# Kernel tuning notes

Hardware: AMD Instinct MI355X
Metric: run time of the kernel (lower is better)

## Reference

```python
import jax, jax.numpy as jnp
import numpy as np

EPS = 1e-5  # torch GroupNorm default

def gn1(x, g, b):
    # GroupNorm with 1 group: normalize over (C,H,W) per sample, per-channel affine
    m = jnp.mean(x, axis=(1, 2, 3), keepdims=True)
    v = jnp.var(x, axis=(1, 2, 3), keepdims=True)
    return (x - m) * jax.lax.rsqrt(v + EPS) * g[None, :, None, None] + b[None, :, None, None]

def conv1x1(x, w):
    # w: [O, C]; 1x1 conv == channel GEMM
    return jnp.einsum('bchw,oc->bohw', x, w)

def interp_bilinear_ac(x, H, W):
    # bilinear, align_corners=True
    b, c, h, w = x.shape
    ys = jnp.linspace(0.0, h - 1.0, H)
    xs = jnp.linspace(0.0, w - 1.0, W)
    y0 = jnp.floor(ys).astype(jnp.int32); y1 = jnp.minimum(y0 + 1, h - 1)
    x0 = jnp.floor(xs).astype(jnp.int32); x1 = jnp.minimum(x0 + 1, w - 1)
    wy = (ys - y0)[None, None, :, None]
    wx = (xs - x0)[None, None, None, :]
    rows = x[:, :, y0, :] * (1.0 - wy) + x[:, :, y1, :] * wy
    return rows[:, :, :, x0] * (1.0 - wx) + rows[:, :, :, x1] * wx

C, KC, NCLS = 256, 128, 21
B, H, W = 8, 128, 128

def setup_inputs() -> dict:
    key = jax.random.key(0)
    ks = jax.random.split(key, 16)
    s = 0.01  # matches torch init normal_(0, 0.01)
    d = {
        'feats': jax.random.normal(ks[0], (B, C, H, W), jnp.float32),
        'out_aux': jax.random.normal(ks[1], (B, NCLS, 64, 64), jnp.float32),
        # f_pixel: conv(C->KC), GN, relu, conv(KC->KC), GN, relu
        'fp_w1': jax.random.normal(ks[2], (KC, C), jnp.float32) * s,
        'fp_g1': jnp.ones((KC,), jnp.float32), 'fp_b1': jnp.zeros((KC,), jnp.float32),
        'fp_w2': jax.random.normal(ks[3], (KC, KC), jnp.float32) * s,
        'fp_g2': jnp.ones((KC,), jnp.float32), 'fp_b2': jnp.zeros((KC,), jnp.float32),
        # f_object
        'fo_w1': jax.random.normal(ks[4], (KC, C), jnp.float32) * s,
        'fo_g1': jnp.ones((KC,), jnp.float32), 'fo_b1': jnp.zeros((KC,), jnp.float32),
        'fo_w2': jax.random.normal(ks[5], (KC, KC), jnp.float32) * s,
        'fo_g2': jnp.ones((KC,), jnp.float32), 'fo_b2': jnp.zeros((KC,), jnp.float32),
        # f_down
        'fd_w': jax.random.normal(ks[6], (KC, C), jnp.float32) * s,
        'fd_g': jnp.ones((KC,), jnp.float32), 'fd_b': jnp.zeros((KC,), jnp.float32),
        # f_up
        'fu_w': jax.random.normal(ks[7], (C, KC), jnp.float32) * s,
        'fu_g': jnp.ones((C,), jnp.float32), 'fu_b': jnp.zeros((C,), jnp.float32),
        # conv_bn_dropout: conv(2C->C), GN, relu (dropout is identity in eval)
        'cb_w': jax.random.normal(ks[8], (C, 2 * C), jnp.float32) * s,
        'cb_g': jnp.ones((C,), jnp.float32), 'cb_b': jnp.zeros((C,), jnp.float32),
    }
    return d

def reference(feats, out_aux, fp_w1, fp_g1, fp_b1, fp_w2, fp_g2, fp_b2,
              fo_w1, fo_g1, fo_b1, fo_w2, fo_g2, fo_b2,
              fd_w, fd_g, fd_b, fu_w, fu_g, fu_b, cb_w, cb_g, cb_b):
    b, c, h, w = feats.shape
    kc = fp_w1.shape[0]
    n = h * w
    # --- SpatialGather: softmax(probs over spatial) @ feats^T -> proxy [b,c,K,1]
    probs = interp_bilinear_ac(out_aux, h, w).reshape(b, -1, n)
    probs = jax.nn.softmax(probs, axis=2)                       # [b,K,n]
    ctx = jnp.einsum('bkn,bcn->bck', probs, feats.reshape(b, c, n))[..., None]  # [b,c,K,1]
    # --- ObjectAttentionBlock2D
    q = jax.nn.relu(gn1(conv1x1(feats, fp_w1), fp_g1, fp_b1))
    q = jax.nn.relu(gn1(conv1x1(q, fp_w2), fp_g2, fp_b2)).reshape(b, kc, n)     # [b,kc,n]
    k = jax.nn.relu(gn1(conv1x1(ctx, fo_w1), fo_g1, fo_b1))
    k = jax.nn.relu(gn1(conv1x1(k, fo_w2), fo_g2, fo_b2)).reshape(b, kc, -1)    # [b,kc,K]
    v = jax.nn.relu(gn1(conv1x1(ctx, fd_w), fd_g, fd_b)).reshape(b, kc, -1)     # [b,kc,K]
    sim = jnp.einsum('bcn,bck->bnk', q, k) * (kc ** -0.5)       # [b,n,K]
    sim = jax.nn.softmax(sim, axis=-1)
    att = jnp.einsum('bnk,bck->bcn', sim, v).reshape(b, kc, h, w)
    up = jax.nn.relu(gn1(conv1x1(att, fu_w), fu_g, fu_b))       # [b,c,h,w]
    # --- fuse (dropout = identity at inference)
    cat = jnp.concatenate([up, feats], axis=1)
    return jax.nn.relu(gn1(conv1x1(cat, cb_w), cb_g, cb_b))
```

## Files before the change

### kernel.cpp

```cpp
#include <hip/hip_runtime.h>
#include <hip/hip_bf16.h>

#define BB 8
#define CC 256
#define KCH 128
#define NCLS 21
#define NN 16384
#define IH 64
#define IW 64
#define GEPS 1e-5f

typedef unsigned short u16;
typedef short v8s __attribute__((ext_vector_type(8)));
typedef u16 v8us __attribute__((ext_vector_type(8)));
typedef float v4f __attribute__((ext_vector_type(4)));

#define OFF_STATS   0u
#define OFF_CTX     64u
#define OFF_KMAT    43072u
#define OFF_VMAT    64576u
#define OFF_WB1     86080u
#define OFF_WB2     102464u
#define OFF_WB3     110656u
#define OFF_WB4     127040u
#define OFF_FEATSB  196608u
#define OFF_POOL    16973824u

__device__ __forceinline__ float bfu2f(u16 u) {
    unsigned int x = ((unsigned int)u) << 16;
    return __uint_as_float(x);
}
__device__ __forceinline__ u16 f2bfu(float f) {
    __hip_bfloat16 h = __float2bfloat16(f);
    return *reinterpret_cast<u16*>(&h);
}

__device__ __forceinline__ float blk_sum(float v, float* red) {
    #pragma unroll
    for (int o = 32; o > 0; o >>= 1) v += __shfl_down(v, o, 64);
    int lane = threadIdx.x & 63, w = threadIdx.x >> 6;
    __syncthreads();
    if (lane == 0) red[w] = v;
    __syncthreads();
    return red[0] + red[1] + red[2] + red[3];
}
__device__ __forceinline__ float blk_max(float v, float* red) {
    #pragma unroll
    for (int o = 32; o > 0; o >>= 1) v = fmaxf(v, __shfl_down(v, o, 64));
    int lane = threadIdx.x & 63, w = threadIdx.x >> 6;
    __syncthreads();
    if (lane == 0) red[w] = v;
    __syncthreads();
    return fmaxf(fmaxf(red[0], red[1]), fmaxf(red[2], red[3]));
}

__global__ __launch_bounds__(256) void conv_weights(
    const float* __restrict__ w1, const float* __restrict__ w2,
    const float* __restrict__ w3, const float* __restrict__ w4,
    u16* __restrict__ o1, u16* __restrict__ o2,
    u16* __restrict__ o3, u16* __restrict__ o4)
{
    int i = blockIdx.x * 256 + threadIdx.x;
    if (i < 32768) o1[i] = f2bfu(w1[i]);
    else if (i < 49152) o2[i - 32768] = f2bfu(w2[i - 32768]);
    else if (i < 81920) o3[i - 49152] = f2bfu(w3[i - 49152]);
    else if (i < 212992) o4[i - 81920] = f2bfu(w4[i - 81920]);
}

__global__ __launch_bounds__(256) void feats_to_nhwc(
    const float* __restrict__ feats, u16* __restrict__ outp)
{
    __shared__ float tile[64][65];
    int b = blockIdx.z, c0 = blockIdx.y * 64, n0 = blockIdx.x * 64;
    int tid = threadIdx.x, tx = tid & 63, ty = tid >> 6;
    #pragma unroll
    for (int r = 0; r < 16; r++) {
        int c = ty * 16 + r;
        tile[c][tx] = feats[((size_t)(b * CC + c0 + c)) * NN + n0 + tx];
    }
    __syncthreads();
    #pragma unroll
    for (int r = 0; r < 16; r++) {
        int nl = ty * 16 + r;
        outp[((size_t)b * NN + n0 + nl) * CC + c0 + tx] = f2bfu(tile[tx][nl]);
    }
}

__global__ __launch_bounds__(256) void interp_softmax_kernel(
    const float* __restrict__ aux, float* __restrict__ probs)
{
    int bk = blockIdx.x;
    const float* src = aux + (size_t)bk * (IH * IW);
    float* dst = probs + (size_t)bk * NN;
    int tid = threadIdx.x;
    __shared__ float red[4];
    const float scale = 63.0f / 127.0f;
    float lmax = -1e30f;
    for (int idx = tid; idx < NN; idx += 256) {
        int y = idx >> 7, x = idx & 127;
        float fy = y * scale, fx = x * scale;
        int y0 = (int)fy, x0 = (int)fx;
        float wy = fy - y0, wx = fx - x0;
        int y1 = min(y0 + 1, IH - 1), x1 = min(x0 + 1, IW - 1);
        float v00 = src[y0 * IW + x0];
        float v01 = src[y0 * IW + x1];
        float v10 = src[y1 * IW + x0];
        float v11 = src[y1 * IW + x1];
        float v = (v00 * (1.f - wx) + v01 * wx) * (1.f - wy)
                + (v10 * (1.f - wx) + v11 * wx) * wy;
        dst[idx] = v;
        lmax = fmaxf(lmax, v);
    }
    float gmax = blk_max(lmax, red);
    float lsum = 0.f;
    for (int idx = tid; idx < NN; idx += 256) {
        float e = __expf(dst[idx] - gmax);
        dst[idx] = e;
        lsum += e;
    }
    float gsum = blk_sum(lsum, red);
    float inv = 1.0f / gsum;
    for (int idx = tid; idx < NN; idx += 256) dst[idx] *= inv;
}

__global__ __launch_bounds__(256) void ctx_kernel(
    const float* __restrict__ feats, const float* __restrict__ probs,
    float* __restrict__ ctx)
{
    int c = blockIdx.x, b = blockIdx.y, tid = threadIdx.x;
    const float* f = feats + ((size_t)(b * CC + c)) * NN;
    const float* p = probs + (size_t)b * NCLS * NN;
    float acc[NCLS];
    #pragma unroll
    for (int k = 0; k < NCLS; k++) acc[k] = 0.f;
    for (int n = tid; n < NN; n += 256) {
        float fv = f[n];
        #pragma unroll
        for (int k = 0; k < NCLS; k++) acc[k] += fv * p[(size_t)k * NN + n];
    }
    __shared__ float red[4 * NCLS];
    int lane = tid & 63, w = tid >> 6;
    #pragma unroll
    for (int k = 0; k < NCLS; k++) {
        float v = acc[k];
        #pragma unroll
        for (int o = 32; o > 0; o >>= 1) v += __shfl_down(v, o, 64);
        if (lane == 0) red[w * NCLS + k] = v;
    }
    __syncthreads();
    if (tid < NCLS) {
        ctx[((size_t)(b * CC + c)) * NCLS + tid] =
            red[tid] + red[NCLS + tid] + red[2 * NCLS + tid] + red[3 * NCLS + tid];
    }
}

__device__ void kv_branch(const float* src, int Cs, const float* W,
                          const float* g, const float* bb, float* dst, float* red)
{
    int tid = threadIdx.x;
    float s = 0.f, s2 = 0.f;
    for (int idx = tid; idx < KCH * NCLS; idx += 256) {
        int o = idx / NCLS, k = idx - o * NCLS;
        const float* wr = W + (size_t)o * Cs;
        float acc = 0.f;
        for (int c = 0; c < Cs; c++) acc += wr[c] * src[c * NCLS + k];
        dst[idx] = acc;
        s += acc; s2 += acc * acc;
    }
    __syncthreads();
    s = blk_sum(s, red);
    s2 = blk_sum(s2, red);
    const float inv = 1.0f / (KCH * NCLS);
    float mean = s * inv;
    float var = s2 * inv - mean * mean;
    float rstd = rsqrtf(var + GEPS);
    for (int idx = tid; idx < KCH * NCLS; idx += 256) {
        int o = idx / NCLS;
        float v = (dst[idx] - mean) * rstd * g[o] + bb[o];
        dst[idx] = fmaxf(v, 0.f);
    }
    __syncthreads();
}

__global__ __launch_bounds__(256) void kv_kernel(
    const float* __restrict__ ctx,
    const float* fo_w1, const float* fo_g1, const float* fo_b1,
    const float* fo_w2, const float* fo_g2, const float* fo_b2,
    const float* fd_w, const float* fd_g, const float* fd_b,
    float* __restrict__ kmat, float* __restrict__ vmat)
{
    __shared__ float sctx[CC * NCLS];
    __shared__ float h1[KCH * NCLS];
    __shared__ float h2[KCH * NCLS];
    __shared__ float red[4];
    int b = blockIdx.x, tid = threadIdx.x;
    for (int i = tid; i < CC * NCLS; i += 256) sctx[i] = ctx[(size_t)b * CC * NCLS + i];
    __syncthreads();
    kv_branch(sctx, CC, fo_w1, fo_g1, fo_b1, h1, red);
    kv_branch(h1, KCH, fo_w2, fo_g2, fo_b2, h2, red);
    for (int i = tid; i < KCH * NCLS; i += 256) kmat[(size_t)b * KCH * NCLS + i] = h2[i];
    kv_branch(sctx, CC, fd_w, fd_g, fd_b, h1, red);
    for (int i = tid; i < KCH * NCLS; i += 256) vmat[(size_t)b * KCH * NCLS + i] = h1[i];
}

template<int KTOT, int K1, bool OUT_BF16>
__global__ __launch_bounds__(256) void mfma_gemm(
    const u16* __restrict__ xa, const u16* __restrict__ xb,
    const u16* __restrict__ wmat, void* __restrict__ outv,
    int Odim, float* __restrict__ ostat)
{
    __shared__ u16 lA[128 * 32];
    __shared__ u16 lB[128 * 32];
    __shared__ float red[8];
    const int b = blockIdx.z;
    const int n0 = blockIdx.x * 128;
    const int o0 = blockIdx.y * 128;
    const int tid = threadIdx.x;
    const int wave = tid >> 6, lane = tid & 63;
    const int quad = lane >> 4, l15 = lane & 15;
    const int wm = (wave & 1) * 64, wn = (wave >> 1) * 64;
    const int srow = lane >> 2;
    const int skc = (lane & 3) * 8;
    const size_t xbase = (size_t)b * NN + n0;

    v4f acc[4][4] = {};

    for (int c0 = 0; c0 < KTOT; c0 += 32) {
        #pragma unroll
        for (int t = 0; t < 2; t++) {
            int inst = wave * 2 + t;
            int row = inst * 16 + srow;
            int cc = c0 + skc;
            const u16* src;
            if (K1 == KTOT || cc < K1)
                src = xa + (xbase + row) * K1 + cc;
            else
                src = xb + (xbase + row) * (KTOT - K1) + (cc - K1);
            v8s v = *(const v8s*)src;
            *(v8s*)&lA[inst * 512 + lane * 8] = v;
        }
        #pragma unroll
        for (int t = 0; t < 2; t++) {
            int inst = wave * 2 + t;
            int row = inst * 16 + srow;
            v8s v = *(const v8s*)(wmat + (size_t)(o0 + row) * KTOT + c0 + skc);
            *(v8s*)&lB[inst * 512 + lane * 8] = v;
        }
        __syncthreads();
        v8s af[4], bfr[4];
        #pragma unroll
        for (int i = 0; i < 4; i++)
            af[i] = *(const v8s*)&lA[(wm + i * 16 + l15) * 32 + quad * 8];
        #pragma unroll
        for (int j = 0; j < 4; j++)
            bfr[j] = *(const v8s*)&lB[(wn + j * 16 + l15) * 32 + quad * 8];
        #pragma unroll
        for (int i = 0; i < 4; i++)
            #pragma unroll
            for (int j = 0; j < 4; j++)
                acc[i][j] = __builtin_amdgcn_mfma_f32_16x16x32_bf16(
                    af[i], bfr[j], acc[i][j], 0, 0, 0);
        __syncthreads();
    }

    float s = 0.f, s2 = 0.f;
    #pragma unroll
    for (int i = 0; i < 4; i++) {
        #pragma unroll
        for (int j = 0; j < 4; j++) {
            #pragma unroll
            for (int r = 0; r < 4; r++) {
                float v = acc[i][j][r];
                int n = n0 + wm + i * 16 + quad * 4 + r;
                int o = o0 + wn + j * 16 + l15;
                size_t addr = ((size_t)b * NN + n) * (size_t)Odim + o;
                if (OUT_BF16) ((u16*)outv)[addr] = f2bfu(v);
                else ((float*)outv)[addr] = v;
                s += v; s2 += v * v;
            }
        }
    }
    #pragma unroll
    for (int o = 32; o > 0; o >>= 1) {
        s += __shfl_down(s, o, 64);
        s2 += __shfl_down(s2, o, 64);
    }
    if (lane == 0) { red[wave] = s; red[4 + wave] = s2; }
    __syncthreads();
    if (tid == 0) {
        atomicAdd(&ostat[2 * b], red[0] + red[1] + red[2] + red[3]);
        atomicAdd(&ostat[2 * b + 1], red[4] + red[5] + red[6] + red[7]);
    }
}

template<bool IN_BF16>
__global__ __launch_bounds__(256) void norm_convert(
    const void* __restrict__ inv, u16* __restrict__ outp,
    const float* __restrict__ stat, float ninv,
    const float* __restrict__ gam, const float* __restrict__ bet,
    int cmask, int bshift8)
{
    size_t f8 = (size_t)blockIdx.x * 256 + threadIdx.x;
    int b = (int)(f8 >> bshift8);
    int c = (int)((f8 * 8) & (size_t)cmask);
    float sm = stat[2 * b], sq = stat[2 * b + 1];
    float mean = sm * ninv;
    float var = sq * ninv - mean * mean;
    float rstd = rsqrtf(var + GEPS);
    float x[8];
    if (IN_BF16) {
        v8us v = ((const v8us*)inv)[f8];
        #pragma unroll
        for (int e = 0; e < 8; e++) x[e] = bfu2f(v[e]);
    } else {
        const float4* p = (const float4*)inv + f8 * 2;
        float4 a = p[0], d = p[1];
        x[0] = a.x; x[1] = a.y; x[2] = a.z; x[3] = a.w;
        x[4] = d.x; x[5] = d.y; x[6] = d.z; x[7] = d.w;
    }
    v8us o;
    #pragma unroll
    for (int e = 0; e < 8; e++) {
        float v = (x[e] - mean) * rstd * gam[c + e] + bet[c + e];
        o[e] = f2bfu(fmaxf(v, 0.f));
    }
    ((v8us*)outp)[f8] = o;
}

__global__ __launch_bounds__(256) void attn_kernel(
    const float* __restrict__ t2, const float* __restrict__ kmat,
    const float* __restrict__ vmat, const float* __restrict__ stat,
    const float* __restrict__ g2, const float* __restrict__ b2,
    u16* __restrict__ att)
{
    __shared__ float sk[KCH * NCLS];
    __shared__ float sv[KCH * NCLS];
    __shared__ float sgam[KCH], sbet[KCH];
    __shared__ float sims[256][NCLS + 1];
    int b = blockIdx.y;
    int n0 = blockIdx.x * 256;
    int tid = threadIdx.x;
    for (int i = tid; i < KCH * NCLS; i += 256) {
        sk[i] = kmat[(size_t)b * KCH * NCLS + i];
        sv[i] = vmat[(size_t)b * KCH * NCLS + i];
    }
    if (tid < KCH) { sgam[tid] = g2[tid]; sbet[tid] = b2[tid]; }
    __syncthreads();
    const float cinv = 1.0f / (128.f * 16384.f);
    float sm = stat[2 * b], sq = stat[2 * b + 1];
    float mean = sm * cinv;
    float var = sq * cinv - mean * mean;
    float rstd = rsqrtf(var + GEPS);

    {
        int n = n0 + tid;
        const float* q = t2 + ((size_t)b * NN + n) * KCH;
        float sim[NCLS] = {};
        for (int c = 0; c < KCH; c += 4) {
            float4 q4 = *(const float4*)(q + c);
            float qv[4] = {q4.x, q4.y, q4.z, q4.w};
            #pragma unroll
            for (int e = 0; e < 4; e++) {
                float qn = fmaxf((qv[e] - mean) * rstd * sgam[c + e] + sbet[c + e], 0.f);
                #pragma unroll
                for (int k = 0; k < NCLS; k++) sim[k] += qn * sk[(c + e) * NCLS + k];
            }
        }
        const float scale = 0.08838834764831845f;
        float m = -1e30f;
        #pragma unroll
        for (int k = 0; k < NCLS; k++) { sim[k] *= scale; m = fmaxf(m, sim[k]); }
        float ssum = 0.f;
        #pragma unroll
        for (int k = 0; k < NCLS; k++) { sim[k] = __expf(sim[k] - m); ssum += sim[k]; }
        float inv = 1.0f / ssum;
        #pragma unroll
        for (int k = 0; k < NCLS; k++) sims[tid][k] = sim[k] * inv;
    }
    __syncthreads();
    int c2 = (tid & 63) * 2;
    int psub = tid >> 6;
    for (int p = psub; p < 256; p += 4) {
        float a0 = 0.f, a1 = 0.f;
        #pragma unroll
        for (int k = 0; k < NCLS; k++) {
            float pr = sims[p][k];
            a0 += pr * sv[c2 * NCLS + k];
            a1 += pr * sv[(c2 + 1) * NCLS + k];
        }
        ushort2 st; st.x = f2bfu(a0); st.y = f2bfu(a1);
        *(ushort2*)&att[((size_t)b * NN + n0 + p) * KCH + c2] = st;
    }
}

__global__ __launch_bounds__(256) void final_kernel(
    const u16* __restrict__ t4, float* __restrict__ outp,
    const float* __restrict__ stat,
    const float* __restrict__ g, const float* __restrict__ bb)
{
    __shared__ float tile[64][65];
    int b = blockIdx.z, c0 = blockIdx.y * 64, n0 = blockIdx.x * 64;
    int tid = threadIdx.x, tx = tid & 63, ty = tid >> 6;
    const float cinv = 1.0f / (256.f * 16384.f);
    float sm = stat[2 * b], sq = stat[2 * b + 1];
    float mean = sm * cinv;
    float var = sq * cinv - mean * mean;
    float rstd = rsqrtf(var + GEPS);
    #pragma unroll
    for (int r = 0; r < 16; r++) {
        int nl = ty * 16 + r;
        tile[nl][tx] = bfu2f(t4[((size_t)b * NN + n0 + nl) * CC + c0 + tx]);
    }
    __syncthreads();
    #pragma unroll
    for (int r = 0; r < 16; r++) {
        int c = c0 + ty * 16 + r;
        float v = (tile[tx][ty * 16 + r] - mean) * rstd * g[c] + bb[c];
        outp[((size_t)(b * CC + c)) * NN + n0 + tx] = fmaxf(v, 0.f);
    }
}

extern "C" void kernel_launch(void* const* d_in, const int* in_sizes, int n_in,
                              void* d_out, int out_size, void* d_ws, size_t ws_size,
                              hipStream_t stream) {
    const float* feats   = (const float*)d_in[0];
    const float* out_aux = (const float*)d_in[1];
    const float* fp_w1 = (const float*)d_in[2];
    const float* fp_g1 = (const float*)d_in[3];
    const float* fp_b1 = (const float*)d_in[4];
    const float* fp_w2 = (const float*)d_in[5];
    const float* fp_g2 = (const float*)d_in[6];
    const float* fp_b2 = (const float*)d_in[7];
    const float* fo_w1 = (const float*)d_in[8];
    const float* fo_g1 = (const float*)d_in[9];
    const float* fo_b1 = (const float*)d_in[10];
    const float* fo_w2 = (const float*)d_in[11];
    const float* fo_g2 = (const float*)d_in[12];
    const float* fo_b2 = (const float*)d_in[13];
    const float* fd_w  = (const float*)d_in[14];
    const float* fd_g  = (const float*)d_in[15];
    const float* fd_b  = (const float*)d_in[16];
    const float* fu_w  = (const float*)d_in[17];
    const float* fu_g  = (const float*)d_in[18];
    const float* fu_b  = (const float*)d_in[19];
    const float* cb_w  = (const float*)d_in[20];
    const float* cb_g  = (const float*)d_in[21];
    const float* cb_b  = (const float*)d_in[22];

    float* ws = (float*)d_ws;
    float* stats = ws + OFF_STATS;
    float* ctx   = ws + OFF_CTX;
    float* kmat  = ws + OFF_KMAT;
    float* vmat  = ws + OFF_VMAT;
    u16* wb1 = (u16*)(ws + OFF_WB1);
    u16* wb2 = (u16*)(ws + OFF_WB2);
    u16* wb3 = (u16*)(ws + OFF_WB3);
    u16* wb4 = (u16*)(ws + OFF_WB4);
    u16* featsb = (u16*)(ws + OFF_FEATSB);
    float* pool = ws + OFF_POOL;
    float* probs = pool;
    float* t1 = pool;
    u16* x2b = (u16*)(pool + 16777216);
    float* t2 = pool;
    u16* attb = (u16*)(pool + 25165824);
    u16* t3b = (u16*)pool;
    u16* x4ab = (u16*)(pool + 16777216);
    u16* t4b = (u16*)pool;
    float* st0 = stats, *st1 = stats + 16, *st2 = stats + 32, *st3 = stats + 48;

    hipMemsetAsync(stats, 0, 64 * sizeof(float), stream);

    conv_weights<<<832, 256, 0, stream>>>(fp_w1, fp_w2, fu_w, cb_w, wb1, wb2, wb3, wb4);
    feats_to_nhwc<<<dim3(NN / 64, CC / 64, BB), 256, 0, stream>>>(feats, featsb);
    interp_softmax_kernel<<<BB * NCLS, 256, 0, stream>>>(out_aux, probs);
    ctx_kernel<<<dim3(CC, BB), 256, 0, stream>>>(feats, probs, ctx);
    kv_kernel<<<BB, 256, 0, stream>>>(ctx, fo_w1, fo_g1, fo_b1, fo_w2, fo_g2, fo_b2,
                                      fd_w, fd_g, fd_b, kmat, vmat);
    mfma_gemm<256, 256, false><<<dim3(NN / 128, 1, BB), 256, 0, stream>>>(
        featsb, nullptr, wb1, t1, KCH, st0);
    norm_convert<false><<<2097152 / 256, 256, 0, stream>>>(
        t1, x2b, st0, 1.f / (KCH * (float)NN), fp_g1, fp_b1, 127, 18);
    mfma_gemm<128, 128, false><<<dim3(NN / 128, 1, BB), 256, 0, stream>>>(
        x2b, nullptr, wb2, t2, KCH, st1);
    attn_kernel<<<dim3(NN / 256, BB), 256, 0, stream>>>(
        t2, kmat, vmat, st1, fp_g2, fp_b2, attb);
    mfma_gemm<128, 128, true><<<dim3(NN / 128, 2, BB), 256, 0, stream>>>(
        attb, nullptr, wb3, t3b, CC, st2);
    norm_convert<true><<<4194304 / 256, 256, 0, stream>>>(
        t3b, x4ab, st2, 1.f / (CC * (float)NN), fu_g, fu_b, 255, 19);
    mfma_gemm<512, 256, true><<<dim3(NN / 128, 2, BB), 256, 0, stream>>>(
        x4ab, featsb, wb4, t4b, CC, st3);
    final_kernel<<<dim3(NN / 64, CC / 64, BB), 256, 0, stream>>>(
        t4b, (float*)d_out, st3, cb_g, cb_b);
}
```

Measured before the change: 915.6 us.

## Split key/value branch kernel across many blocks with atomic GroupNorm stats

The single 8-block kv_kernel, which ran both the key and value branches serially per batch, is split into kv1 (key and value first conv in parallel over 11x2x8 blocks) and kv2 (second key conv). GroupNorm statistics are accumulated with atomics, and the final normalisation and ReLU for k and v move into attn_kernel's shared-memory load. The goal is to remove a badly under-parallelised serial kernel from the critical path, at the cost of an extra launch and redundant ctx loads into shared memory per block.

```diff
diff --git a/kernel.cpp b/kernel.cpp
--- a/kernel.cpp
+++ b/kernel.cpp
@@ -16,13 +16,13 @@
 typedef float v4f __attribute__((ext_vector_type(4)));
 
 #define OFF_STATS   0u
-#define OFF_CTX     64u
-#define OFF_KMAT    43072u
-#define OFF_VMAT    64576u
-#define OFF_WB1     86080u
-#define OFF_WB2     102464u
-#define OFF_WB3     110656u
-#define OFF_WB4     127040u
+#define OFF_CTX     128u
+#define OFF_KMAT    43136u
+#define OFF_VMAT    64640u
+#define OFF_WB1     86144u
+#define OFF_WB2     102528u
+#define OFF_WB3     110720u
+#define OFF_WB4     127104u
 #define OFF_FEATSB  196608u
 #define OFF_POOL    16973824u
 
@@ -52,6 +52,22 @@
     if (lane == 0) red[w] = v;
     __syncthreads();
     return fmaxf(fmaxf(red[0], red[1]), fmaxf(red[2], red[3]));
+}
+
+__device__ __forceinline__ void stat_atomic(float s, float s2, float* target) {
+    __shared__ float r2[8];
+    #pragma unroll
+    for (int o = 32; o > 0; o >>= 1) {
+        s += __shfl_down(s, o, 64);
+        s2 += __shfl_down(s2, o, 64);
+    }
+    int lane = threadIdx.x & 63, w = threadIdx.x >> 6;
+    if (lane == 0) { r2[w] = s; r2[4 + w] = s2; }
+    __syncthreads();
+    if (threadIdx.x == 0) {
+        atomicAdd(&target[0], r2[0] + r2[1] + r2[2] + r2[3]);
+        atomicAdd(&target[1], r2[4] + r2[5] + r2[6] + r2[7]);
+    }
 }
 
 __global__ __launch_bounds__(256) void conv_weights(
@@ -154,53 +170,64 @@
     }
 }
 
-__device__ void kv_branch(const float* src, int Cs, const float* W,
-                          const float* g, const float* bb, float* dst, float* red)
-{
-    int tid = threadIdx.x;
+__global__ __launch_bounds__(256) void kv1_kernel(
+    const float* __restrict__ ctx, const float* __restrict__ fo_w1,
+    const float* __restrict__ fd_w,
+    float* __restrict__ h1raw, float* __restrict__ v1raw,
+    float* __restrict__ kvstat)
+{
+    __shared__ float sctx[CC * NCLS];
+    int b = blockIdx.z, br = blockIdx.y, tid = threadIdx.x;
+    for (int i = tid; i < CC * NCLS; i += 256)
+        sctx[i] = ctx[(size_t)b * CC * NCLS + i];
+    __syncthreads();
+    int idx = blockIdx.x * 256 + tid;
+    const float* W = br ? fd_w : fo_w1;
+    float* dst = br ? v1raw : h1raw;
     float s = 0.f, s2 = 0.f;
-    for (int idx = tid; idx < KCH * NCLS; idx += 256) {
+    if (idx < KCH * NCLS) {
         int o = idx / NCLS, k = idx - o * NCLS;
-        const float* wr = W + (size_t)o * Cs;
+        const float* w = W + (size_t)o * CC;
         float acc = 0.f;
-        for (int c = 0; c < Cs; c++) acc += wr[c] * src[c * NCLS + k];
-        dst[idx] = acc;
-        s += acc; s2 += acc * acc;
-    }
-    __syncthreads();
-    s = blk_sum(s, red);
-    s2 = blk_sum(s2, red);
-    const float inv = 1.0f / (KCH * NCLS);
-    float mean = s * inv;
-    float var = s2 * inv - mean * mean;
+        #pragma unroll 4
+        for (int c = 0; c < CC; c++) acc += w[c] * sctx[c * NCLS + k];
+        dst[(size_t)b * KCH * NCLS + idx] = acc;
+        s = acc; s2 = acc * acc;
+    }
+    stat_atomic(s, s2, &kvstat[(br * 8 + b) * 2]);
+}
+
+__global__ __launch_bounds__(256) void kv2_kernel(
+    const float* __restrict__ h1raw, const float* __restrict__ fo_w2,
+    const float* __restrict__ g1, const float* __restrict__ b1,
+    const float* __restrict__ st_in, float* __restrict__ h2raw,
+    float* __restrict__ st_out)
+{
+    __shared__ float sh[KCH * NCLS];
+    int b = blockIdx.z, tid = threadIdx.x;
+    const float ninv = 1.0f / (KCH * NCLS);
+    float sm = st_in[b * 2], sq = st_in[b * 2 + 1];
+    float mean = sm * ninv;
+    float var = sq * ninv - mean * mean;
     float rstd = rsqrtf(var + GEPS);
-    for (int idx = tid; idx < KCH * NCLS; idx += 256) {
-        int o = idx / NCLS;
-        float v = (dst[idx] - mean) * rstd * g[o] + bb[o];
-        dst[idx] = fmaxf(v, 0.f);
-    }
-    __syncthreads();
-}
-
-__global__ __launch_bounds__(256) void kv_kernel(
-    const float* __restrict__ ctx,
-    const float* fo_w1, const float* fo_g1, const float* fo_b1,
-    const float* fo_w2, const float* fo_g2, const float* fo_b2,
-    const float* fd_w, const float* fd_g, const float* fd_b,
-    float* __restrict__ kmat, float* __restrict__ vmat)
-{
-    __shared__ float sctx[CC * NCLS];
-    __shared__ float h1[KCH * NCLS];
-    __shared__ float h2[KCH * NCLS];
-    __shared__ float red[4];
-    int b = blockIdx.x, tid = threadIdx.x;
-    for (int i = tid; i < CC * NCLS; i += 256) sctx[i] = ctx[(size_t)b * CC * NCLS + i];
-    __syncthreads();
-    kv_branch(sctx, CC, fo_w1, fo_g1, fo_b1, h1, red);
-    kv_branch(h1, KCH, fo_w2, fo_g2, fo_b2, h2, red);
-    for (int i = tid; i < KCH * NCLS; i += 256) kmat[(size_t)b * KCH * NCLS + i] = h2[i];
-    kv_branch(sctx, CC, fd_w, fd_g, fd_b, h1, red);
-    for (int i = tid; i < KCH * NCLS; i += 256) vmat[(size_t)b * KCH * NCLS + i] = h1[i];
+    for (int i = tid; i < KCH * NCLS; i += 256) {
+        int c = i / NCLS;
+        float v = (h1raw[(size_t)b * KCH * NCLS + i] - mean) * rstd * g1[c] + b1[c];
+        sh[i] = fmaxf(v, 0.f);
+    }
+    __syncthreads();
+    int idx = blockIdx.x * 256 + tid;
+    float s = 0.f, s2 = 0.f;
+    if (idx < KCH * NCLS) {
+        int o = idx / NCLS, k = idx - o * NCLS;
+        const float* w = fo_w2 + (size_t)o * KCH;
+        float acc = 0.f;
+        #pragma unroll 4
+        for (int c = 0; c < KCH; c++) acc += w[c] * sh[c * NCLS + k];
+        h2raw[(size_t)b * KCH * NCLS + idx] = acc;
+        s = acc; s2 = acc * acc;
+    }
+    stat_atomic(s, s2, &st_out[b * 2]);
 }
 
 template<int KTOT, int K1, bool OUT_BF16>
@@ -328,9 +355,13 @@
 }
 
 __global__ __launch_bounds__(256) void attn_kernel(
-    const float* __restrict__ t2, const float* __restrict__ kmat,
-    const float* __restrict__ vmat, const float* __restrict__ stat,
+    const float* __restrict__ t2, const float* __restrict__ kraw,
+    const float* __restrict__ vraw, const float* __restrict__ stat,
     const float* __restrict__ g2, const float* __restrict__ b2,
+    const float* __restrict__ stK, const float* __restrict__ ko_g,
+    const float* __restrict__ ko_b,
+    const float* __restrict__ stV, const float* __restrict__ vd_g,
+    const float* __restrict__ vd_b,
     u16* __restrict__ att)
 {
     __shared__ float sk[KCH * NCLS];
@@ -340,9 +371,18 @@
     int b = blockIdx.y;
     int n0 = blockIdx.x * 256;
     int tid = threadIdx.x;
+    const float kvinv = 1.0f / (KCH * NCLS);
+    float km = stK[b * 2] * kvinv;
+    float kv2_ = stK[b * 2 + 1] * kvinv;
+    float krs = rsqrtf(kv2_ - km * km + GEPS);
+    float vm = stV[b * 2] * kvinv;
+    float vv2 = stV[b * 2 + 1] * kvinv;
+    float vrs = rsqrtf(vv2 - vm * vm + GEPS);
     for (int i = tid; i < KCH * NCLS; i += 256) {
-        sk[i] = kmat[(size_t)b * KCH * NCLS + i];
-        sv[i] = vmat[(size_t)b * KCH * NCLS + i];
+        int c = i / NCLS;
+        size_t base = (size_t)b * KCH * NCLS + i;
+        sk[i] = fmaxf((kraw[base] - km) * krs * ko_g[c] + ko_b[c], 0.f);
+        sv[i] = fmaxf((vraw[base] - vm) * vrs * vd_g[c] + vd_b[c], 0.f);
     }
     if (tid < KCH) { sgam[tid] = g2[tid]; sbet[tid] = b2[tid]; }
     __syncthreads();
@@ -459,6 +499,7 @@
     u16* featsb = (u16*)(ws + OFF_FEATSB);
     float* pool = ws + OFF_POOL;
     float* probs = pool;
+    float* h1raw = pool;
     float* t1 = pool;
     u16* x2b = (u16*)(pool + 16777216);
     float* t2 = pool;
@@ -467,15 +508,18 @@
     u16* x4ab = (u16*)(pool + 16777216);
     u16* t4b = (u16*)pool;
     float* st0 = stats, *st1 = stats + 16, *st2 = stats + 32, *st3 = stats + 48;
-
-    hipMemsetAsync(stats, 0, 64 * sizeof(float), stream);
+    float* stK1 = stats + 64, *stV = stats + 80, *stK2 = stats + 96;
+
+    hipMemsetAsync(stats, 0, 128 * sizeof(float), stream);
 
     conv_weights<<<832, 256, 0, stream>>>(fp_w1, fp_w2, fu_w, cb_w, wb1, wb2, wb3, wb4);
     feats_to_nhwc<<<dim3(NN / 64, CC / 64, BB), 256, 0, stream>>>(feats, featsb);
     interp_softmax_kernel<<<BB * NCLS, 256, 0, stream>>>(out_aux, probs);
     ctx_kernel<<<dim3(CC, BB), 256, 0, stream>>>(feats, probs, ctx);
-    kv_kernel<<<BB, 256, 0, stream>>>(ctx, fo_w1, fo_g1, fo_b1, fo_w2, fo_g2, fo_b2,
-                                      fd_w, fd_g, fd_b, kmat, vmat);
+    kv1_kernel<<<dim3(11, 2, BB), 256, 0, stream>>>(
+        ctx, fo_w1, fd_w, h1raw, vmat, stK1);
+    kv2_kernel<<<dim3(11, 1, BB), 256, 0, stream>>>(
+        h1raw, fo_w2, fo_g1, fo_b1, stK1, kmat, stK2);
     mfma_gemm<256, 256, false><<<dim3(NN / 128, 1, BB), 256, 0, stream>>>(
         featsb, nullptr, wb1, t1, KCH, st0);
     norm_convert<false><<<2097152 / 256, 256, 0, stream>>>(
@@ -483,7 +527,8 @@
     mfma_gemm<128, 128, false><<<dim3(NN / 128, 1, BB), 256, 0, stream>>>(
         x2b, nullptr, wb2, t2, KCH, st1);
     attn_kernel<<<dim3(NN / 256, BB), 256, 0, stream>>>(
-        t2, kmat, vmat, st1, fp_g2, fp_b2, attb);
+        t2, kmat, vmat, st1, fp_g2, fp_b2,
+        stK2, fo_g2, fo_b2, stV, fd_g, fd_b, attb);
     mfma_gemm<128, 128, true><<<dim3(NN / 128, 2, BB), 256, 0, stream>>>(
         attb, nullptr, wb3, t3b, CC, st2);
     norm_convert<true><<<4194304 / 256, 256, 0, stream>>>(
```

New measurement: 791.2 us. 1.16x faster.
